# Kernel optimization log

Measured on AMD Instinct MI355X. Metric: run time of the kernel, lower is better.

The kernel has to match this reference:

```python
import jax, jax.numpy as jnp
import numpy as np

HIDDEN = 32
INPUT = 4
OUT = 1


def _gru_layer(x, W_ih, W_hh, b_ih, b_hh):
    # x: [B, S, in]; W_ih: [3H, in]; W_hh: [3H, H]; biases: [3H]
    B, S, _ = x.shape
    H = W_hh.shape[1]
    # precompute input projections for all timesteps (one big GEMM)
    xg = jnp.einsum('bsi,gi->bsg', x, W_ih) + b_ih  # [B, S, 3H]
    xg_t = jnp.swapaxes(xg, 0, 1)  # [S, B, 3H] for scan

    def step(h, xg_s):
        hg = h @ W_hh.T + b_hh  # [B, 3H]
        xr, xz, xn = jnp.split(xg_s, 3, axis=-1)
        hr, hz, hn = jnp.split(hg, 3, axis=-1)
        r = jax.nn.sigmoid(xr + hr)
        z = jax.nn.sigmoid(xz + hz)
        n = jnp.tanh(xn + r * hn)
        h_new = (1.0 - z) * n + z * h
        return h_new, h_new

    h0 = jnp.zeros((B, H), dtype=x.dtype)
    _, ys = jax.lax.scan(step, h0, xg_t)  # ys: [S, B, H]
    return jnp.swapaxes(ys, 0, 1)  # [B, S, H]


def setup_inputs() -> dict:
    key = jax.random.key(0)
    ks = jax.random.split(key, 14)
    s_in = 1.0 / np.sqrt(HIDDEN)
    u = lambda k, shp: jax.random.uniform(k, shp, jnp.float32, -s_in, s_in)
    x = jax.random.normal(ks[0], (4096, 512, INPUT), dtype=jnp.float32)
    return {
        'x': x,
        'W_ih0': u(ks[1], (3 * HIDDEN, INPUT)),
        'W_hh0': u(ks[2], (3 * HIDDEN, HIDDEN)),
        'b_ih0': u(ks[3], (3 * HIDDEN,)),
        'b_hh0': u(ks[4], (3 * HIDDEN,)),
        'W_ih1': u(ks[5], (3 * HIDDEN, HIDDEN)),
        'W_hh1': u(ks[6], (3 * HIDDEN, HIDDEN)),
        'b_ih1': u(ks[7], (3 * HIDDEN,)),
        'b_hh1': u(ks[8], (3 * HIDDEN,)),
        'W_fc2': u(ks[9], (HIDDEN, HIDDEN)),
        'b_fc2': u(ks[10], (HIDDEN,)),
        'W_fc': u(ks[11], (OUT, HIDDEN)),
        'b_fc': u(ks[12], (OUT,)),
    }


def reference(x, W_ih0, W_hh0, b_ih0, b_hh0, W_ih1, W_hh1, b_ih1, b_hh1,
              W_fc2, b_fc2, W_fc, b_fc):
    # 2-layer GRU (h0 = zeros; dropout inactive at inference)
    h1 = _gru_layer(x, W_ih0, W_hh0, b_ih0, b_hh0)   # [B, S, H]
    h2 = _gru_layer(h1, W_ih1, W_hh1, b_ih1, b_hh1)  # [B, S, H]
    last = h2[:, -1, :]                              # [B, H]
    out = last @ W_fc2.T + b_fc2                     # [B, H]
    out = out @ W_fc.T + b_fc                        # [B, 1]
    return out
```

## Files before the change

kernel.cpp:

```cpp
#include <hip/hip_runtime.h>


#define SEQ 512
#define LOG2E 1.44269504088896340736f

typedef __attribute__((ext_vector_type(8))) short  short8;
typedef __attribute__((ext_vector_type(4))) float  f32x4;
typedef __attribute__((ext_vector_type(2))) unsigned uint2v;

static __device__ __forceinline__ unsigned short f2bf(float f) {
    unsigned u = __builtin_bit_cast(unsigned, f);
    return (unsigned short)((u + 0x7fffu + ((u >> 16) & 1u)) >> 16);
}
static __device__ __forceinline__ float bf2f(unsigned short b) {
    return __builtin_bit_cast(float, ((unsigned)b) << 16);
}
static __device__ __forceinline__ unsigned cvtpk(float a, float b) {
    unsigned r;
    asm("v_cvt_pk_bf16_f32 %0, %1, %2" : "=v"(r) : "v"(a), "v"(b));
    return r;
}
static __device__ __forceinline__ float sigm(float x) {
    return __builtin_amdgcn_rcpf(1.0f + __builtin_amdgcn_exp2f(-LOG2E * x));
}
static __device__ __forceinline__ float tanh_(float x) {
    return 1.0f - 2.0f * __builtin_amdgcn_rcpf(1.0f + __builtin_amdgcn_exp2f((2.0f * LOG2E) * x));
}

#define MFMA(A, B, C) __builtin_amdgcn_mfma_f32_16x16x32_bf16((A), (B), (C), 0, 0, 0)

static __device__ __forceinline__ f32x4 side2(short8 Wh, short8 Wl, short8 B,
                                              f32x4 Cin) {
    f32x4 a = MFMA(Wh, B, Cin);
    a = MFMA(Wl, B, a);
    return a;
}

static __device__ __forceinline__ void cvt8(const float* p, short8& h8, short8& l8) {
    f32x4 v0 = *(const f32x4*)p;
    f32x4 v1 = *(const f32x4*)(p + 4);
#pragma unroll
    for (int e = 0; e < 8; ++e) {
        float v = (e < 4) ? v0[e] : v1[e - 4];
        unsigned short hb = f2bf(v);
        h8[e] = (short)hb;
        l8[e] = (short)f2bf(v - bf2f(hb));
    }
}

__global__ __launch_bounds__(512, 1) void gru_fused(
    const float* __restrict__ x,
    const float* __restrict__ Wih0, const float* __restrict__ Whh0,
    const float* __restrict__ bih0, const float* __restrict__ bhh0,
    const float* __restrict__ Wih1, const float* __restrict__ Whh1,
    const float* __restrict__ bih1, const float* __restrict__ bhh1,
    const float* __restrict__ Wfc2, const float* __restrict__ bfc2,
    const float* __restrict__ Wfc,  const float* __restrict__ bfc,
    float* __restrict__ out)
{
    const int tid  = threadIdx.x;
    const int lane = tid & 63;
    const int wid  = tid >> 6;
    const int role = wid >> 2;
    const int L    = (wid >> 1) & 1;
    const int hf   = wid & 1;
    const int c    = lane & 15;
    const int q    = lane >> 4;
    const int b0   = blockIdx.x * 16;

    __shared__ __align__(16) char smem[38016];
    char*  ST01 = smem;
    char*  ST2  = smem + 2560;
    f32x4* XS   = (f32x4*)(smem + 5120);
    f32x4* AX0  = (f32x4*)(smem + 13312);
    f32x4* AX1  = (f32x4*)(smem + 25600);
    float* EP   = (float*)(smem + 37888);

    for (int i = tid; i < 1280; i += 512) ((unsigned*)smem)[i] = 0u;

    if (tid < 256) {
        const int row = tid & 15, so = tid >> 4;
#pragma unroll
        for (int k = 0; k < 2; ++k) {
            const int step = so + 16 * k;
            XS[step * 16 + row] =
                *(const f32x4*)(x + ((long)(b0 + row) * SEQ + step) * 4);
        }
    }

    const int tts[3] = {hf, 2 + hf, 4 + hf};

    short8 whhh[3], whhl[3];
    f32x4  bhv2 = {0, 0, 0, 0};
    f32x4  wx0[12];
    float  bxs[12];
    short8 wuh[3], wul[3];
    f32x4  bxv[3];

    if (role == 0) {
        const float* Whp = L ? Whh1 : Whh0;
        const float* bhp = L ? bhh1 : bhh0;
#pragma unroll
        for (int j = 0; j < 3; ++j)
            cvt8(Whp + (16 * tts[j] + c) * 32 + 8 * q, whhh[j], whhl[j]);
        bhv2 = *(const f32x4*)(bhp + 16 * tts[2] + 4 * q);
    } else if (L == 0) {
#pragma unroll
        for (int j = 0; j < 3; ++j)
#pragma unroll
            for (int r = 0; r < 4; ++r) {
                const int g = 16 * tts[j] + 4 * q + r;
                wx0[4 * j + r] = *(const f32x4*)(Wih0 + g * 4);
                bxs[4 * j + r] = bih0[g] + ((j < 2) ? bhh0[g] : 0.0f);
            }
    } else {
#pragma unroll
        for (int j = 0; j < 3; ++j) {
            cvt8(Wih1 + (16 * tts[j] + c) * 32 + 8 * q, wuh[j], wul[j]);
            f32x4 bb = *(const f32x4*)(bih1 + 16 * tts[j] + 4 * q);
            if (j < 2) bb += *(const f32x4*)(bhh1 + 16 * tts[j] + 4 * q);
            bxv[j] = bb;
        }
    }

    if (role == 1 && L == 0) {
        f32x4 xv = *(const f32x4*)(x + (long)(b0 + c) * (SEQ * 4));
#pragma unroll
        for (int j = 0; j < 3; ++j) {
            f32x4 a;
#pragma unroll
            for (int r = 0; r < 4; ++r) {
                f32x4 w = wx0[4 * j + r];
                a[r] = bxs[4 * j + r] + w[0] * xv[0] + w[1] * xv[1]
                     + w[2] * xv[2] + w[3] * xv[3];
            }
            AX0[tts[j] * 64 + q * 16 + c] = a;
        }
    }

    float hst[4] = {0, 0, 0, 0};
    const int frag_off = c * 80 + q * 16;
    const int wr_off   = c * 80 + (16 * hf + 4 * q) * 2;

    __syncthreads();

#pragma unroll 2
    for (int i = 0; i <= SEQ + 1; ++i) {
        if (role == 0) {
            const bool act = (L == 0) ? (i < SEQ) : (i >= 2);
            if (act) {
                const char*  st;
                const f32x4* axb;
                char*        dst;
                if (L == 0) {
                    st  = ST01 + ((i + 1) & 1) * 1280;
                    axb = AX0 + (i & 1) * 384;
                    dst = ST01 + (i & 1) * 1280;
                } else {
                    st  = ST2 + ((i + 1) & 1) * 1280;
                    axb = AX1 + ((i + 1) & 1) * 384;
                    dst = ST2 + (i & 1) * 1280;
                }
                short8 sfrag = *(const short8*)(st + frag_off);
                f32x4 ax0v = axb[tts[0] * 64 + q * 16 + c];
                f32x4 ax1v = axb[tts[1] * 64 + q * 16 + c];
                f32x4 ax2v = axb[tts[2] * 64 + q * 16 + c];

                f32x4 p0 = side2(whhh[0], whhl[0], sfrag, ax0v);
                f32x4 p1 = side2(whhh[1], whhl[1], sfrag, ax1v);
                f32x4 p2 = side2(whhh[2], whhl[2], sfrag, bhv2);

                float hv[4];
#pragma unroll
                for (int r = 0; r < 4; ++r) {
                    float rg = sigm(p0[r]);
                    float zg = sigm(p1[r]);
                    float ng = tanh_(ax2v[r] + rg * p2[r]);
                    float hN = ng + zg * (hst[r] - ng);
                    hst[r] = hN;
                    hv[r] = hN;
                }
                unsigned w0 = cvtpk(hv[0], hv[1]);
                unsigned w1 = cvtpk(hv[2], hv[3]);
                uint2v wpk = {w0, w1};
                *(uint2v*)(dst + wr_off) = wpk;
            }
        } else if (L == 0) {
            if ((i & 15) == 0) {
                const int base = i + 16;
                if (base < SEQ) {
                    const int hidx = tid - 256;
                    const int row = hidx & 15, so = hidx >> 4;
#pragma unroll
                    for (int k = 0; k < 2; ++k) {
                        const int step = base + so + 8 * k;
                        XS[(step & 31) * 16 + row] =
                            *(const f32x4*)(x + ((long)(b0 + row) * SEQ + step) * 4);
                    }
                }
            }
            const int step = i + 1;
            if (step < SEQ) {
                f32x4 xv = XS[(step & 31) * 16 + c];
                f32x4* dstax = AX0 + (step & 1) * 384;
#pragma unroll
                for (int j = 0; j < 3; ++j) {
                    f32x4 a;
#pragma unroll
                    for (int r = 0; r < 4; ++r) {
                        f32x4 w = wx0[4 * j + r];
                        a[r] = bxs[4 * j + r] + w[0] * xv[0] + w[1] * xv[1]
                             + w[2] * xv[2] + w[3] * xv[3];
                    }
                    dstax[tts[j] * 64 + q * 16 + c] = a;
                }
            }
        } else {
            if (i <= SEQ) {
                const char* us = ST01 + ((i + 1) & 1) * 1280;
                short8 uf = *(const short8*)(us + frag_off);
                f32x4* dstax = AX1 + (i & 1) * 384;
#pragma unroll
                for (int j = 0; j < 3; ++j) {
                    f32x4 a = side2(wuh[j], wul[j], uf, bxv[j]);
                    dstax[tts[j] * 64 + q * 16 + c] = a;
                }
            }
        }
        __syncthreads();
    }

    if (role == 0 && L == 1) {
        float we[4] = {0, 0, 0, 0};
        const float* w2p = Wfc2 + 16 * hf + 4 * q;
#pragma unroll 8
        for (int j = 0; j < 32; ++j) {
            float wf = Wfc[j];
            f32x4 w2 = *(const f32x4*)(w2p + j * 32);
#pragma unroll
            for (int r = 0; r < 4; ++r) we[r] += wf * w2[r];
        }
        float acc = we[0] * hst[0] + we[1] * hst[1] + we[2] * hst[2] + we[3] * hst[3];
        acc += __shfl_xor(acc, 16);
        acc += __shfl_xor(acc, 32);
        if (q == 0) EP[hf * 16 + c] = acc;
    }
    __syncthreads();
    if (wid == 0 && q == 0) {
        float cst = bfc[0];
        for (int j = 0; j < 32; ++j) cst += Wfc[j] * bfc2[j];
        out[b0 + c] = EP[c] + EP[16 + c] + cst;
    }
}

extern "C" void kernel_launch(void* const* d_in, const int* in_sizes, int n_in,
                              void* d_out, int out_size, void* d_ws, size_t ws_size,
                              hipStream_t stream) {
    const float* x    = (const float*)d_in[0];
    const float* Wih0 = (const float*)d_in[1];
    const float* Whh0 = (const float*)d_in[2];
    const float* bih0 = (const float*)d_in[3];
    const float* bhh0 = (const float*)d_in[4];
    const float* Wih1 = (const float*)d_in[5];
    const float* Whh1 = (const float*)d_in[6];
    const float* bih1 = (const float*)d_in[7];
    const float* bhh1 = (const float*)d_in[8];
    const float* Wfc2 = (const float*)d_in[9];
    const float* bfc2 = (const float*)d_in[10];
    const float* Wfc  = (const float*)d_in[11];
    const float* bfc  = (const float*)d_in[12];

    const int nblocks = out_size / 16;
    hipLaunchKernelGGL(gru_fused, dim3(nblocks), dim3(512), 0, stream,
                       x, Wih0, Whh0, bih0, bhh0, Wih1, Whh1, bih1, bhh1,
                       Wfc2, bfc2, Wfc, bfc, (float*)d_out);
}
```

Measured before the change: 221.2 us.

## Merge helper waves into two and prioritize recurrence waves with setprio

The block shrinks from 8 to 6 waves. Two helper waves now compute both the layer-0 input projection and the layer-1 input MFMA projection, and they prefetch x in smaller, more frequent chunks. The main recurrence waves raise their scheduling priority during the gate computation, and the candidate-gate MFMA is issued first. The aim is cheaper per-step block barriers and less contention for the critical serial path, at the risk of longer helper work per step stalling the barrier.

```diff
diff --git a/kernel.cpp b/kernel.cpp
--- a/kernel.cpp
+++ b/kernel.cpp
@@ -48,7 +48,7 @@
     }
 }
 
-__global__ __launch_bounds__(512, 1) void gru_fused(
+__global__ __launch_bounds__(384, 1) void gru_fused(
     const float* __restrict__ x,
     const float* __restrict__ Wih0, const float* __restrict__ Whh0,
     const float* __restrict__ bih0, const float* __restrict__ bhh0,
@@ -61,7 +61,7 @@
     const int tid  = threadIdx.x;
     const int lane = tid & 63;
     const int wid  = tid >> 6;
-    const int role = wid >> 2;
+    const bool isMain = (wid < 4);
     const int L    = (wid >> 1) & 1;
     const int hf   = wid & 1;
     const int c    = lane & 15;
@@ -76,44 +76,38 @@
     f32x4* AX1  = (f32x4*)(smem + 25600);
     float* EP   = (float*)(smem + 37888);
 
-    for (int i = tid; i < 1280; i += 512) ((unsigned*)smem)[i] = 0u;
-
-    if (tid < 256) {
-        const int row = tid & 15, so = tid >> 4;
-#pragma unroll
-        for (int k = 0; k < 2; ++k) {
-            const int step = so + 16 * k;
-            XS[step * 16 + row] =
-                *(const f32x4*)(x + ((long)(b0 + row) * SEQ + step) * 4);
-        }
+    for (int i = tid; i < 1280; i += 384) ((unsigned*)smem)[i] = 0u;
+
+    for (int e = tid; e < 512; e += 384) {
+        const int step = e >> 4, row = e & 15;
+        XS[e] = *(const f32x4*)(x + ((long)(b0 + row) * SEQ + step) * 4);
     }
 
     const int tts[3] = {hf, 2 + hf, 4 + hf};
 
-    short8 whhh[3], whhl[3];
+    short8 whh_[3], whl_[3];
     f32x4  bhv2 = {0, 0, 0, 0};
-    f32x4  wx0[12];
+    f32x4  wx[12];
     float  bxs[12];
     short8 wuh[3], wul[3];
     f32x4  bxv[3];
 
-    if (role == 0) {
+    if (isMain) {
         const float* Whp = L ? Whh1 : Whh0;
         const float* bhp = L ? bhh1 : bhh0;
 #pragma unroll
         for (int j = 0; j < 3; ++j)
-            cvt8(Whp + (16 * tts[j] + c) * 32 + 8 * q, whhh[j], whhl[j]);
+            cvt8(Whp + (16 * tts[j] + c) * 32 + 8 * q, whh_[j], whl_[j]);
         bhv2 = *(const f32x4*)(bhp + 16 * tts[2] + 4 * q);
-    } else if (L == 0) {
+    } else {
 #pragma unroll
         for (int j = 0; j < 3; ++j)
 #pragma unroll
             for (int r = 0; r < 4; ++r) {
                 const int g = 16 * tts[j] + 4 * q + r;
-                wx0[4 * j + r] = *(const f32x4*)(Wih0 + g * 4);
+                wx[4 * j + r]  = *(const f32x4*)(Wih0 + g * 4);
                 bxs[4 * j + r] = bih0[g] + ((j < 2) ? bhh0[g] : 0.0f);
             }
-    } else {
 #pragma unroll
         for (int j = 0; j < 3; ++j) {
             cvt8(Wih1 + (16 * tts[j] + c) * 32 + 8 * q, wuh[j], wul[j]);
@@ -121,16 +115,13 @@
             if (j < 2) bb += *(const f32x4*)(bhh1 + 16 * tts[j] + 4 * q);
             bxv[j] = bb;
         }
-    }
-
-    if (role == 1 && L == 0) {
         f32x4 xv = *(const f32x4*)(x + (long)(b0 + c) * (SEQ * 4));
 #pragma unroll
         for (int j = 0; j < 3; ++j) {
             f32x4 a;
 #pragma unroll
             for (int r = 0; r < 4; ++r) {
-                f32x4 w = wx0[4 * j + r];
+                f32x4 w = wx[4 * j + r];
                 a[r] = bxs[4 * j + r] + w[0] * xv[0] + w[1] * xv[1]
                      + w[2] * xv[2] + w[3] * xv[3];
             }
@@ -146,9 +137,10 @@
 
 #pragma unroll 2
     for (int i = 0; i <= SEQ + 1; ++i) {
-        if (role == 0) {
+        if (isMain) {
             const bool act = (L == 0) ? (i < SEQ) : (i >= 2);
             if (act) {
+                __builtin_amdgcn_s_setprio(1);
                 const char*  st;
                 const f32x4* axb;
                 char*        dst;
@@ -166,9 +158,9 @@
                 f32x4 ax1v = axb[tts[1] * 64 + q * 16 + c];
                 f32x4 ax2v = axb[tts[2] * 64 + q * 16 + c];
 
-                f32x4 p0 = side2(whhh[0], whhl[0], sfrag, ax0v);
-                f32x4 p1 = side2(whhh[1], whhl[1], sfrag, ax1v);
-                f32x4 p2 = side2(whhh[2], whhl[2], sfrag, bhv2);
+                f32x4 p2 = side2(whh_[2], whl_[2], sfrag, bhv2);
+                f32x4 p0 = side2(whh_[0], whl_[0], sfrag, ax0v);
+                f32x4 p1 = side2(whh_[1], whl_[1], sfrag, ax1v);
 
                 float hv[4];
 #pragma unroll
@@ -184,53 +176,48 @@
                 unsigned w1 = cvtpk(hv[2], hv[3]);
                 uint2v wpk = {w0, w1};
                 *(uint2v*)(dst + wr_off) = wpk;
-            }
-        } else if (L == 0) {
-            if ((i & 15) == 0) {
+                __builtin_amdgcn_s_setprio(0);
+            }
+        } else {
+            if ((i & 7) == 0) {
                 const int base = i + 16;
                 if (base < SEQ) {
-                    const int hidx = tid - 256;
-                    const int row = hidx & 15, so = hidx >> 4;
-#pragma unroll
-                    for (int k = 0; k < 2; ++k) {
-                        const int step = base + so + 8 * k;
-                        XS[(step & 31) * 16 + row] =
-                            *(const f32x4*)(x + ((long)(b0 + row) * SEQ + step) * 4);
-                    }
-                }
-            }
-            const int step = i + 1;
-            if (step < SEQ) {
-                f32x4 xv = XS[(step & 31) * 16 + c];
-                f32x4* dstax = AX0 + (step & 1) * 384;
+                    const int idx = (wid - 4) * 64 + lane;
+                    const int step = base + (idx >> 4), row = idx & 15;
+                    XS[(step & 31) * 16 + row] =
+                        *(const f32x4*)(x + ((long)(b0 + row) * SEQ + step) * 4);
+                }
+            }
+            if (i >= 1 && i <= SEQ) {
+                const char* us = ST01 + ((i + 1) & 1) * 1280;
+                short8 uf = *(const short8*)(us + frag_off);
+                f32x4* dstax = AX1 + (i & 1) * 384;
+#pragma unroll
+                for (int j = 0; j < 3; ++j)
+                    dstax[tts[j] * 64 + q * 16 + c] =
+                        side2(wuh[j], wul[j], uf, bxv[j]);
+            }
+            const int stp = i + 1;
+            if (stp < SEQ) {
+                f32x4 xv = XS[(stp & 31) * 16 + c];
+                f32x4* dstax = AX0 + (stp & 1) * 384;
 #pragma unroll
                 for (int j = 0; j < 3; ++j) {
                     f32x4 a;
 #pragma unroll
                     for (int r = 0; r < 4; ++r) {
-                        f32x4 w = wx0[4 * j + r];
+                        f32x4 w = wx[4 * j + r];
                         a[r] = bxs[4 * j + r] + w[0] * xv[0] + w[1] * xv[1]
                              + w[2] * xv[2] + w[3] * xv[3];
                     }
                     dstax[tts[j] * 64 + q * 16 + c] = a;
                 }
             }
-        } else {
-            if (i <= SEQ) {
-                const char* us = ST01 + ((i + 1) & 1) * 1280;
-                short8 uf = *(const short8*)(us + frag_off);
-                f32x4* dstax = AX1 + (i & 1) * 384;
-#pragma unroll
-                for (int j = 0; j < 3; ++j) {
-                    f32x4 a = side2(wuh[j], wul[j], uf, bxv[j]);
-                    dstax[tts[j] * 64 + q * 16 + c] = a;
-                }
-            }
         }
         __syncthreads();
     }
 
-    if (role == 0 && L == 1) {
+    if (isMain && L == 1) {
         float we[4] = {0, 0, 0, 0};
         const float* w2p = Wfc2 + 16 * hf + 4 * q;
 #pragma unroll 8
@@ -271,7 +258,7 @@
     const float* bfc  = (const float*)d_in[12];
 
     const int nblocks = out_size / 16;
-    hipLaunchKernelGGL(gru_fused, dim3(nblocks), dim3(512), 0, stream,
+    hipLaunchKernelGGL(gru_fused, dim3(nblocks), dim3(384), 0, stream,
                        x, Wih0, Whh0, bih0, bhh0, Wih1, Whh1, bih1, bhh1,
                        Wfc2, bfc2, Wfc, bfc, (float*)d_out);
 }
```

After: 234.6 us. 6.1% more time.
